# Kernel optimization log

Hardware: AMD Instinct MI355X
Metric: run time of the kernel (lower is better)

Reference implementation:

```python
import jax, jax.numpy as jnp
import numpy as np

L, H, C, V, T_MAX = 12, 12, 768, 50257, 1024
D = C // H
LN_EPS = 1e-5


def layer_norm(x, w, b):
    m = jnp.mean(x, axis=-1, keepdims=True)
    v = jnp.mean(jnp.square(x - m), axis=-1, keepdims=True)
    return (x - m) * jax.lax.rsqrt(v + LN_EPS) * w + b


def setup_inputs() -> dict:
    key = jax.random.key(0)
    ks = jax.random.split(key, 16)
    B, T = 2, 1024
    s = 0.02
    inp = {
        "idx": jax.random.randint(ks[0], (B, T), 0, V),
        "wte": jax.random.normal(ks[1], (V, C), jnp.float32) * s,
        "wpe": jax.random.normal(ks[2], (T_MAX, C), jnp.float32) * s,
        # stacked per-layer params, leading axis = layer
        "ln1_w": jnp.ones((L, C), jnp.float32),
        "ln1_b": jnp.zeros((L, C), jnp.float32),
        "Wq": jax.random.normal(ks[3], (L, C, C), jnp.float32) * s,
        "bq": jnp.zeros((L, C), jnp.float32),
        "Wk": jax.random.normal(ks[4], (L, C, C), jnp.float32) * s,
        "bk": jnp.zeros((L, C), jnp.float32),
        "Wv": jax.random.normal(ks[5], (L, C, C), jnp.float32) * s,
        "bv": jnp.zeros((L, C), jnp.float32),
        "Wo": jax.random.normal(ks[6], (L, C, C), jnp.float32) * (s / np.sqrt(2 * L)),
        "bo": jnp.zeros((L, C), jnp.float32),
        "ln2_w": jnp.ones((L, C), jnp.float32),
        "ln2_b": jnp.zeros((L, C), jnp.float32),
        "Wfc": jax.random.normal(ks[7], (L, C, 4 * C), jnp.float32) * s,
        "bfc": jnp.zeros((L, 4 * C), jnp.float32),
        "Wpr": jax.random.normal(ks[8], (L, 4 * C, C), jnp.float32) * (s / np.sqrt(2 * L)),
        "bpr": jnp.zeros((L, C), jnp.float32),
        "ln_f_w": jnp.ones((C,), jnp.float32),
        "ln_f_b": jnp.zeros((C,), jnp.float32),
        "Wlm": jax.random.normal(ks[9], (C, V), jnp.float32) * s,
    }
    return inp


def _forward(idx, wte, wpe, ln1_w, ln1_b, Wq, bq, Wk, bk, Wv, bv, Wo, bo,
             ln2_w, ln2_b, Wfc, bfc, Wpr, bpr, ln_f_w, ln_f_b, Wlm):
    B, T = idx.shape
    x = wte[idx] + wpe[jnp.arange(T)][None, :, :]  # (B,T,C)
    causal = jnp.tril(jnp.ones((T, T), bool))  # (T,T) causal mask
    scale = 1.0 / np.sqrt(D)
    neg_inf = jnp.finfo(x.dtype).min

    def block(x, p):
        (l1w, l1b, wq, bq_, wk, bk_, wv, bv_, wo, bo_,
         l2w, l2b, wfc, bfc_, wpr, bpr_) = p
        h = layer_norm(x, l1w, l1b)
        q = (h @ wq + bq_).reshape(B, T, H, D)
        k = (h @ wk + bk_).reshape(B, T, H, D)
        v = (h @ wv + bv_).reshape(B, T, H, D)
        scores = jnp.einsum("bqhd,bkhd->bhqk", q, k) * scale
        scores = jnp.where(causal[None, None], scores, neg_inf)
        attn = jax.nn.softmax(scores, axis=-1)
        y = jnp.einsum("bhqk,bkhd->bqhd", attn, v).reshape(B, T, C)
        x = x + y @ wo + bo_
        h2 = layer_norm(x, l2w, l2b)
        x = x + jax.nn.gelu(h2 @ wfc + bfc_, approximate=False) @ wpr + bpr_
        return x, None

    params = (ln1_w, ln1_b, Wq, bq, Wk, bk, Wv, bv, Wo, bo,
              ln2_w, ln2_b, Wfc, bfc, Wpr, bpr)
    x, _ = jax.lax.scan(block, x, params)
    x = layer_norm(x, ln_f_w, ln_f_b)
    logits = x @ Wlm  # (B,T,V)
    return logits


def reference(idx, wte, wpe, ln1_w, ln1_b, Wq, bq, Wk, bk, Wv, bv, Wo, bo,
              ln2_w, ln2_b, Wfc, bfc, Wpr, bpr, ln_f_w, ln_f_b, Wlm):
    return _forward(idx, wte, wpe, ln1_w, ln1_b, Wq, bq, Wk, bk, Wv, bv, Wo, bo,
                    ln2_w, ln2_b, Wfc, bfc, Wpr, bpr, ln_f_w, ln_f_b, Wlm)
```

## Files before the change

### kernel.cpp

```cpp
#include <hip/hip_runtime.h>
#include <math.h>
#include <cstddef>


#define Cdim 768
#define Hn   12
#define Ln   12
#define Tn   1024
#define Bn   2
#define Mrows (Bn * Tn)

typedef unsigned short ushort_t;
typedef __bf16 bf16x8 __attribute__((ext_vector_type(8)));
typedef float  f32x4  __attribute__((ext_vector_type(4)));

__device__ __forceinline__ ushort_t f2bf(float v) {
    union { float f; unsigned int u; } x; x.f = v;
    unsigned int r = x.u + 0x7fffu + ((x.u >> 16) & 1u);
    return (ushort_t)(r >> 16);
}
__device__ __forceinline__ float gelu_f(float v) {
    return 0.5f * v * (1.0f + erff(v * 0.70710678118654752f));
}
__device__ __forceinline__ void gload16(const void* g, void* l) {
    __builtin_amdgcn_global_load_lds(
        (const __attribute__((address_space(1))) unsigned int*)g,
        (__attribute__((address_space(3))) unsigned int*)l, 16, 0, 0);
}

__global__ void embed_k(const int* __restrict__ idx, const float* __restrict__ wte,
                        const float* __restrict__ wpe, float* __restrict__ x) {
    int i = blockIdx.x * 256 + threadIdx.x;
    int c  = i % Cdim;
    int bt = i / Cdim;
    int t  = bt % Tn;
    int tok = idx[bt];
    x[i] = wte[(size_t)tok * Cdim + c] + wpe[(size_t)t * Cdim + c];
}

__global__ __launch_bounds__(256) void ln_k(const float* __restrict__ x,
                                            const float* __restrict__ w,
                                            const float* __restrict__ b,
                                            ushort_t* __restrict__ out) {
    int row = blockIdx.x;
    const float* xr = x + (size_t)row * Cdim;
    int t = threadIdx.x;
    float v0 = xr[t], v1 = xr[t + 256], v2 = xr[t + 512];
    float s = v0 + v1 + v2;
    #pragma unroll
    for (int o = 32; o > 0; o >>= 1) s += __shfl_xor(s, o);
    __shared__ float red[8];
    int wid = t >> 6;
    if ((t & 63) == 0) red[wid] = s;
    __syncthreads();
    float mean = (red[0] + red[1] + red[2] + red[3]) * (1.0f / 768.0f);
    float d0 = v0 - mean, d1 = v1 - mean, d2 = v2 - mean;
    float sq = d0 * d0 + d1 * d1 + d2 * d2;
    #pragma unroll
    for (int o = 32; o > 0; o >>= 1) sq += __shfl_xor(sq, o);
    if ((t & 63) == 0) red[4 + wid] = sq;
    __syncthreads();
    float var = (red[4] + red[5] + red[6] + red[7]) * (1.0f / 768.0f);
    float rstd = rsqrtf(var + 1e-5f);
    ushort_t* orow = out + (size_t)row * Cdim;
    orow[t]       = f2bf(d0 * rstd * w[t]       + b[t]);
    orow[t + 256] = f2bf(d1 * rstd * w[t + 256] + b[t + 256]);
    orow[t + 512] = f2bf(d2 * rstd * w[t + 512] + b[t + 512]);
}

__device__ __forceinline__ void tconv_tile(const float* __restrict__ W,
                                           ushort_t* __restrict__ WT,
                                           int K, int N, int n0, int k0, bool guard) {
    __shared__ float t[32][33];
    int x = threadIdx.x & 31, y = threadIdx.x >> 5;
    #pragma unroll
    for (int j = 0; j < 4; ++j) {
        int kk = k0 + y + j * 8, nn = n0 + x;
        t[y + j * 8][x] = (!guard || nn < N) ? W[(size_t)kk * N + nn] : 0.0f;
    }
    __syncthreads();
    #pragma unroll
    for (int j = 0; j < 4; ++j) {
        int nn = n0 + y + j * 8, kk = k0 + x;
        WT[(size_t)nn * K + kk] = f2bf(t[x][y + j * 8]);
    }
}

__global__ __launch_bounds__(256) void wconv_k(const float* __restrict__ W,
                                               ushort_t* __restrict__ WT,
                                               int K, int N) {
    tconv_tile(W, WT, K, N, blockIdx.x * 32, blockIdx.y * 32, true);
}

__global__ __launch_bounds__(256) void conv_layer_k(
    const float* __restrict__ Wq, const float* __restrict__ Wk,
    const float* __restrict__ Wv, const float* __restrict__ Wo,
    const float* __restrict__ Wfc, const float* __restrict__ Wpr,
    const float* __restrict__ bq, const float* __restrict__ bk,
    const float* __restrict__ bv,
    ushort_t* __restrict__ wqkvt, ushort_t* __restrict__ wot,
    ushort_t* __restrict__ wfct,  ushort_t* __restrict__ wprt,
    float* __restrict__ bqkv) {
    int bid = blockIdx.x;
    if (bid < 2304) {
        int z = bid / 576, t = bid % 576;
        const float* W = (z == 0) ? Wq : (z == 1) ? Wk : (z == 2) ? Wv : Wo;
        ushort_t* dst = (z < 3) ? (wqkvt + (size_t)z * 768 * 768) : wot;
        tconv_tile(W, dst, 768, 768, (t % 24) * 32, (t / 24) * 32, false);
    } else if (bid < 4608) {
        int t = bid - 2304;
        tconv_tile(Wfc, wfct, 768, 3072, (t % 96) * 32, (t / 96) * 32, false);
    } else if (bid < 6912) {
        int t = bid - 4608;
        tconv_tile(Wpr, wprt, 3072, 768, (t % 24) * 32, (t / 24) * 32, false);
    } else {
        int i = (bid - 6912) * 256 + threadIdx.x;
        bqkv[i] = (i < 768) ? bq[i] : (i < 1536 ? bk[i - 768] : bv[i - 1536]);
    }
}

template <bool BIAS, bool GELU_, bool RES, bool OUTBF16>
__global__ __launch_bounds__(256) void gemm_bf16_k(
    const ushort_t* __restrict__ A, const ushort_t* __restrict__ Bt,
    const float* __restrict__ bias, const float* __restrict__ res,
    void* __restrict__ Cout, int M, int N, int K) {
    __shared__ ushort_t Alds[2][128 * 32];
    __shared__ ushort_t Blds[2][128 * 32];
    const int tid = threadIdx.x;
    const int lane = tid & 63;
    const int w = tid >> 6;
    const int wr = w >> 1, wc = w & 1;
    const int m0 = blockIdx.y * 128;
    const int n0 = blockIdx.x * 128;

    f32x4 acc[4][4] = {};
    const int srow = w * 32 + (lane >> 2);
    const int skoff = (lane & 3) * 8;
    const ushort_t* Ab = A  + (size_t)(m0 + srow) * K + skoff;
    const ushort_t* Bb = Bt + (size_t)(n0 + srow) * K + skoff;
    char* Al0 = (char*)&Alds[0][0] + (w * 2048 + lane * 16);
    char* Al1 = (char*)&Alds[1][0] + (w * 2048 + lane * 16);
    char* Bl0 = (char*)&Blds[0][0] + (w * 2048 + lane * 16);
    char* Bl1 = (char*)&Blds[1][0] + (w * 2048 + lane * 16);

    const int nk = K >> 6;
    for (int kb = 0; kb < nk; ++kb) {
        const int k0 = kb << 6;
        __syncthreads();
        gload16(Ab + k0,                       Al0);
        gload16(Ab + k0 + (size_t)16 * K,      Al0 + 1024);
        gload16(Ab + k0 + 32,                  Al1);
        gload16(Ab + k0 + 32 + (size_t)16 * K, Al1 + 1024);
        gload16(Bb + k0,                       Bl0);
        gload16(Bb + k0 + (size_t)16 * K,      Bl0 + 1024);
        gload16(Bb + k0 + 32,                  Bl1);
        gload16(Bb + k0 + 32 + (size_t)16 * K, Bl1 + 1024);
        __syncthreads();
        #pragma unroll
        for (int h = 0; h < 2; ++h) {
            bf16x8 af[4], bfr[4];
            #pragma unroll
            for (int i = 0; i < 4; ++i) {
                af[i]  = *(const bf16x8*)((const char*)&Alds[h][0] +
                           ((wr * 64 + i * 16 + (lane & 15)) * 64 + (lane >> 4) * 16));
                bfr[i] = *(const bf16x8*)((const char*)&Blds[h][0] +
                           ((wc * 64 + i * 16 + (lane & 15)) * 64 + (lane >> 4) * 16));
            }
            #pragma unroll
            for (int mi = 0; mi < 4; ++mi)
                #pragma unroll
                for (int ni = 0; ni < 4; ++ni)
                    acc[mi][ni] = __builtin_amdgcn_mfma_f32_16x16x32_bf16(
                        af[mi], bfr[ni], acc[mi][ni], 0, 0, 0);
        }
    }
    const int r0 = (lane >> 4) * 4;
    const int c0 = lane & 15;
    #pragma unroll
    for (int mi = 0; mi < 4; ++mi) {
        #pragma unroll
        for (int ni = 0; ni < 4; ++ni) {
            int col = n0 + wc * 64 + ni * 16 + c0;
            if (col < N) {
                #pragma unroll
                for (int q = 0; q < 4; ++q) {
                    int row = m0 + wr * 64 + mi * 16 + r0 + q;
                    float v = acc[mi][ni][q];
                    if (BIAS) v += bias[col];
                    if (GELU_) v = gelu_f(v);
                    if (RES) v += res[(size_t)row * N + col];
                    if (OUTBF16) ((ushort_t*)Cout)[(size_t)row * N + col] = f2bf(v);
                    else         ((float*)Cout)[(size_t)row * N + col] = v;
                }
            }
        }
    }
}

__global__ __launch_bounds__(512, 2) void gemm_lm_k(
    const ushort_t* __restrict__ A,
    const ushort_t* __restrict__ Bt,
    float* __restrict__ Cout,
    int M, int N, int K, int cpx) {
    __shared__ ushort_t Asl[2][256 * 64];
    __shared__ ushort_t Bsl[2][256 * 64];
    const int tid = threadIdx.x;
    const int lane = tid & 63;
    const int w = tid >> 6;
    const int wr = w >> 2, wc = w & 3;
    const int lid = ((int)blockIdx.x & 7) * cpx + ((int)blockIdx.x >> 3);
    const int m0 = (lid & 7) * 256;
    const int n0 = (lid >> 3) * 256;

    f32x4 acc[8][4] = {};

    const int srow = tid >> 3;
    const int scol = ((tid & 7) * 8) ^ (((tid >> 5) & 1) << 4);
    const ushort_t* Asrc = A  + (size_t)(m0 + srow) * K + scol;
    const ushort_t* Bsrc = Bt + (size_t)(n0 + srow) * K + scol;
    const int ldsoff = tid * 16;

    const int nt = K >> 6;
    #pragma unroll
    for (int j = 0; j < 4; ++j) {
        gload16(Asrc + (size_t)(j * 64) * K, (char*)&Asl[0][0] + ldsoff + j * 8192);
        gload16(Bsrc + (size_t)(j * 64) * K, (char*)&Bsl[0][0] + ldsoff + j * 8192);
    }
    for (int t = 0; t < nt; ++t) {
        const int buf = t & 1;
        if (t + 1 < nt) {
            const int k0 = (t + 1) << 6;
            #pragma unroll
            for (int j = 0; j < 4; ++j) {
                gload16(Asrc + k0 + (size_t)(j * 64) * K,
                        (char*)&Asl[buf ^ 1][0] + ldsoff + j * 8192);
                gload16(Bsrc + k0 + (size_t)(j * 64) * K,
                        (char*)&Bsl[buf ^ 1][0] + ldsoff + j * 8192);
            }
            asm volatile("s_waitcnt vmcnt(8)" ::: "memory");
        } else {
            asm volatile("s_waitcnt vmcnt(0)" ::: "memory");
        }
        __builtin_amdgcn_sched_barrier(0);
        __builtin_amdgcn_s_barrier();
        asm volatile("" ::: "memory");

        const char* Ab = (const char*)&Asl[buf][0];
        const char* Bb = (const char*)&Bsl[buf][0];
        bf16x8 bfr[4][2];
        #pragma unroll
        for (int n = 0; n < 4; ++n)
            #pragma unroll
            for (int ks = 0; ks < 2; ++ks) {
                int row = wc * 64 + n * 16 + (lane & 15);
                int o = row * 128 + ks * 64 + ((lane >> 4) * 16);
                o ^= ((row >> 2) & 1) << 5;
                bfr[n][ks] = *(const bf16x8*)(Bb + o);
            }
        __builtin_amdgcn_s_setprio(1);
        #pragma unroll
        for (int m = 0; m < 8; ++m) {
            bf16x8 af[2];
            #pragma unroll
            for (int ks = 0; ks < 2; ++ks) {
                int row = wr * 128 + m * 16 + (lane & 15);
                int o = row * 128 + ks * 64 + ((lane >> 4) * 16);
                o ^= ((row >> 2) & 1) << 5;
                af[ks] = *(const bf16x8*)(Ab + o);
            }
            #pragma unroll
            for (int n = 0; n < 4; ++n)
                #pragma unroll
                for (int ks = 0; ks < 2; ++ks)
                    acc[m][n] = __builtin_amdgcn_mfma_f32_16x16x32_bf16(
                        af[ks], bfr[n][ks], acc[m][n], 0, 0, 0);
        }
        __builtin_amdgcn_s_setprio(0);
        asm volatile("" ::: "memory");
        __builtin_amdgcn_sched_barrier(0);
        __builtin_amdgcn_s_barrier();
    }

    const int r0 = (lane >> 4) * 4, c0 = lane & 15;
    #pragma unroll
    for (int m = 0; m < 8; ++m)
        #pragma unroll
        for (int n = 0; n < 4; ++n) {
            int col = n0 + wc * 64 + n * 16 + c0;
            if (col < N) {
                #pragma unroll
                for (int q = 0; q < 4; ++q) {
                    int row = m0 + wr * 128 + m * 16 + r0 + q;
                    Cout[(size_t)row * N + col] = acc[m][n][q];
                }
            }
        }
}

template <bool BIAS, bool RES>
__global__ __launch_bounds__(256) void gemm64_k(
    const ushort_t* __restrict__ A, const ushort_t* __restrict__ Bt,
    const float* __restrict__ bias, const float* __restrict__ res,
    float* __restrict__ Cout, int M, int N, int K) {
    __shared__ ushort_t Alds[4][64 * 32];
    __shared__ ushort_t Blds[4][64 * 32];
    const int tid = threadIdx.x;
    const int lane = tid & 63;
    const int w = tid >> 6;
    const int wr = w >> 1, wc = w & 1;
    const int m0 = blockIdx.y * 64;
    const int n0 = blockIdx.x * 64;

    f32x4 acc[2][2] = {};
    const int srow = w * 16 + (lane >> 2);
    const int skoff = (lane & 3) * 8;
    const ushort_t* Ab = A  + (size_t)(m0 + srow) * K + skoff;
    const ushort_t* Bb = Bt + (size_t)(n0 + srow) * K + skoff;

    const int nk = K >> 7;
    for (int kb = 0; kb < nk; ++kb) {
        const int k0 = kb << 7;
        __syncthreads();
        #pragma unroll
        for (int s = 0; s < 4; ++s) {
            gload16(Ab + k0 + s * 32, (char*)&Alds[s][0] + (w * 1024 + lane * 16));
            gload16(Bb + k0 + s * 32, (char*)&Blds[s][0] + (w * 1024 + lane * 16));
        }
        __syncthreads();
        #pragma unroll
        for (int s = 0; s < 4; ++s) {
            bf16x8 af[2], bfr[2];
            #pragma unroll
            for (int i = 0; i < 2; ++i) {
                af[i]  = *(const bf16x8*)((const char*)&Alds[s][0] +
                           ((wr * 32 + i * 16 + (lane & 15)) * 64 + (lane >> 4) * 16));
                bfr[i] = *(const bf16x8*)((const char*)&Blds[s][0] +
                           ((wc * 32 + i * 16 + (lane & 15)) * 64 + (lane >> 4) * 16));
            }
            #pragma unroll
            for (int mi = 0; mi < 2; ++mi)
                #pragma unroll
                for (int ni = 0; ni < 2; ++ni)
                    acc[mi][ni] = __builtin_amdgcn_mfma_f32_16x16x32_bf16(
                        af[mi], bfr[ni], acc[mi][ni], 0, 0, 0);
        }
    }
    const int r0 = (lane >> 4) * 4;
    const int c0 = lane & 15;
    #pragma unroll
    for (int mi = 0; mi < 2; ++mi)
        #pragma unroll
        for (int ni = 0; ni < 2; ++ni) {
            int col = n0 + wc * 32 + ni * 16 + c0;
            #pragma unroll
            for (int q = 0; q < 4; ++q) {
                int row = m0 + wr * 32 + mi * 16 + r0 + q;
                float v = acc[mi][ni][q];
                if (BIAS) v += bias[col];
                if (RES) v += res[(size_t)row * N + col];
                Cout[(size_t)row * N + col] = v;
            }
        }
}

__global__ __launch_bounds__(256) void kvprep_k(const ushort_t* __restrict__ qkvb,
                                                ushort_t* __restrict__ kpb,
                                                ushort_t* __restrict__ vtb) {
    __shared__ ushort_t Ls[256][72];
    const int tc = blockIdx.x, h = blockIdx.y, b = blockIdx.z;
    const int tid = threadIdx.x;
    const int tok = tc * 256 + tid;
    const ushort_t* base = qkvb + (size_t)(b * Tn + tok) * 2304 + h * 64;
    ushort_t* kdst = kpb + ((size_t)(b * Hn + h) * Tn + tok) * 64;
    #pragma unroll
    for (int i = 0; i < 8; ++i)
        *(uint4*)&kdst[i * 8] = *(const uint4*)(base + 768 + i * 8);
    #pragma unroll
    for (int i = 0; i < 8; ++i)
        *(uint4*)&Ls[tid][i * 8] = *(const uint4*)(base + 1536 + i * 8);
    __syncthreads();
    const int d = tid & 63, tg = tid >> 6;
    ushort_t tmp[64];
    #pragma unroll
    for (int i = 0; i < 64; ++i) tmp[i] = Ls[tg * 64 + i][d];
    ushort_t* dst = vtb + ((size_t)(b * Hn + h) * 64 + d) * Tn + tc * 256 + tg * 64;
    #pragma unroll
    for (int i = 0; i < 8; ++i)
        *(uint4*)&dst[i * 8] = *(const uint4*)&tmp[i * 8];
}

__global__ __launch_bounds__(256) void attn_mfma_k(
    const ushort_t* __restrict__ qkvb,
    const ushort_t* __restrict__ kpb,
    const ushort_t* __restrict__ vtb,
    ushort_t* __restrict__ yb) {
    __shared__ ushort_t Ks[64][72];
    __shared__ ushort_t Vt[64][72];
    __shared__ ushort_t Pl[4][16][72];
    const int chunk = (Tn / 64 - 1) - blockIdx.x;
    const int h = blockIdx.y, b = blockIdx.z;
    const int tid = threadIdx.x, lane = tid & 63, w = tid >> 6;
    const int c = lane & 15, g = lane >> 4;
    const int qrow0 = chunk * 64 + w * 16;

    const ushort_t* qp = qkvb + (size_t)(b * Tn + qrow0 + c) * 2304 + h * 64 + g * 8;
    bf16x8 qa0 = *(const bf16x8*)qp;
    bf16x8 qa1 = *(const bf16x8*)(qp + 32);

    f32x4 accO[4] = {};
    float mrun[4], lrun[4];
    #pragma unroll
    for (int q = 0; q < 4; ++q) { mrun[q] = -1e30f; lrun[q] = 0.0f; }

    const int skey = tid >> 2, sd0 = (tid & 3) * 16;
    const ushort_t* ksrc = kpb + ((size_t)(b * Hn + h) * Tn + skey) * 64 + sd0;
    const int vd = tid >> 2, vseg = tid & 3;
    const ushort_t* vsrc = vtb + ((size_t)(b * Hn + h) * 64 + vd) * Tn + vseg * 16;
    ushort_t* KsW = &Ks[skey][sd0];
    ushort_t* VtW = &Vt[vd][vseg * 16];

    const int ntiles = chunk + 1;
    for (int kt = 0; kt < ntiles; ++kt) {
        __syncthreads();
        {
            const ushort_t* kp = ksrc + (size_t)kt * 64 * 64;
            *(uint4*)KsW       = *(const uint4*)kp;
            *(uint4*)(KsW + 8) = *(const uint4*)(kp + 8);
            const ushort_t* vp = vsrc + kt * 64;
            *(uint4*)VtW       = *(const uint4*)vp;
            *(uint4*)(VtW + 8) = *(const uint4*)(vp + 8);
        }
        __syncthreads();

        f32x4 sf[4];
        #pragma unroll
        for (int nk = 0; nk < 4; ++nk) {
            bf16x8 kf0 = *(const bf16x8*)&Ks[nk * 16 + c][g * 8];
            bf16x8 kf1 = *(const bf16x8*)&Ks[nk * 16 + c][g * 8 + 32];
            f32x4 z = {};
            z = __builtin_amdgcn_mfma_f32_16x16x32_bf16(qa0, kf0, z, 0, 0, 0);
            z = __builtin_amdgcn_mfma_f32_16x16x32_bf16(qa1, kf1, z, 0, 0, 0);
            sf[nk] = z;
        }
        float pmax[4] = {-1e30f, -1e30f, -1e30f, -1e30f};
        #pragma unroll
        for (int nk = 0; nk < 4; ++nk) {
            int key = kt * 64 + nk * 16 + c;
            #pragma unroll
            for (int q = 0; q < 4; ++q) {
                float sv = sf[nk][q];
                int row = qrow0 + g * 4 + q;
                sv = (key > row) ? -1e30f : sv;
                sf[nk][q] = sv;
                pmax[q] = fmaxf(pmax[q], sv);
            }
        }
        #pragma unroll
        for (int q = 0; q < 4; ++q)
            #pragma unroll
            for (int off = 1; off < 16; off <<= 1)
                pmax[q] = fmaxf(pmax[q], __shfl_xor(pmax[q], off));
        float corr[4], psum[4];
        #pragma unroll
        for (int q = 0; q < 4; ++q) {
            float mn = fmaxf(mrun[q], pmax[q]);
            corr[q] = __expf((mrun[q] - mn) * 0.125f);
            mrun[q] = mn;
            psum[q] = 0.0f;
        }
        #pragma unroll
        for (int nk = 0; nk < 4; ++nk)
            #pragma unroll
            for (int q = 0; q < 4; ++q) {
                float p = __expf((sf[nk][q] - mrun[q]) * 0.125f);
                psum[q] += p;
                Pl[w][g * 4 + q][nk * 16 + c] = f2bf(p);
            }
        #pragma unroll
        for (int q = 0; q < 4; ++q) {
            #pragma unroll
            for (int off = 1; off < 16; off <<= 1)
                psum[q] += __shfl_xor(psum[q], off);
            lrun[q] = lrun[q] * corr[q] + psum[q];
        }
        #pragma unroll
        for (int ni = 0; ni < 4; ++ni)
            #pragma unroll
            for (int q = 0; q < 4; ++q)
                accO[ni][q] *= corr[q];

        asm volatile("" ::: "memory");
        bf16x8 pa0 = *(const bf16x8*)&Pl[w][c][g * 8];
        bf16x8 pa1 = *(const bf16x8*)&Pl[w][c][g * 8 + 32];
        #pragma unroll
        for (int ni = 0; ni < 4; ++ni) {
            bf16x8 bv0 = *(const bf16x8*)&Vt[ni * 16 + c][g * 8];
            bf16x8 bv1 = *(const bf16x8*)&Vt[ni * 16 + c][g * 8 + 32];
            accO[ni] = __builtin_amdgcn_mfma_f32_16x16x32_bf16(pa0, bv0, accO[ni], 0, 0, 0);
            accO[ni] = __builtin_amdgcn_mfma_f32_16x16x32_bf16(pa1, bv1, accO[ni], 0, 0, 0);
        }
    }

    #pragma unroll
    for (int q = 0; q < 4; ++q) {
        float inv = 1.0f / lrun[q];
        ushort_t* yr = yb + (size_t)(b * Tn + qrow0 + g * 4 + q) * Cdim + h * 64;
        #pragma unroll
        for (int ni = 0; ni < 4; ++ni)
            yr[ni * 16 + c] = f2bf(accO[ni][q] * inv);
    }
}

extern "C" void kernel_launch(void* const* d_in, const int* in_sizes, int n_in,
                              void* d_out, int out_size, void* d_ws, size_t ws_size,
                              hipStream_t stream) {
    const int*   idx  = (const int*)d_in[0];
    const float* wte  = (const float*)d_in[1];
    const float* wpe  = (const float*)d_in[2];
    const float* ln1w = (const float*)d_in[3];
    const float* ln1b = (const float*)d_in[4];
    const float* Wq   = (const float*)d_in[5];
    const float* bq   = (const float*)d_in[6];
    const float* Wk   = (const float*)d_in[7];
    const float* bk   = (const float*)d_in[8];
    const float* Wv   = (const float*)d_in[9];
    const float* bv   = (const float*)d_in[10];
    const float* Wo   = (const float*)d_in[11];
    const float* bo   = (const float*)d_in[12];
    const float* ln2w = (const float*)d_in[13];
    const float* ln2b = (const float*)d_in[14];
    const float* Wfc  = (const float*)d_in[15];
    const float* bfc  = (const float*)d_in[16];
    const float* Wpr  = (const float*)d_in[17];
    const float* bpr  = (const float*)d_in[18];
    const float* lnfw = (const float*)d_in[19];
    const float* lnfb = (const float*)d_in[20];
    const float* Wlm  = (const float*)d_in[21];
    float* out = (float*)d_out;

    const int M = Mrows;
    const int V = out_size / M;
    const int Vpad = ((V + 255) / 256) * 256;

    float*    x     = (float*)d_ws;
    float*    bqkv  = x + (size_t)M * Cdim;
    ushort_t* qkvb  = (ushort_t*)(bqkv + 2304);
    ushort_t* kpb   = qkvb + (size_t)M * 2304;
    ushort_t* vtb   = kpb + (size_t)Bn * Hn * Tn * 64;
    ushort_t* hb    = vtb + (size_t)Bn * Hn * 64 * Tn;
    ushort_t* yb    = hb + (size_t)M * Cdim;
    ushort_t* mid   = yb + (size_t)M * Cdim;
    ushort_t* wqkvt = mid + (size_t)M * 3072;
    ushort_t* wot   = wqkvt + (size_t)2304 * Cdim;
    ushort_t* wfct  = wot + (size_t)Cdim * Cdim;
    ushort_t* wprt  = wfct + (size_t)3072 * Cdim;
    ushort_t* wlmt  = wprt + (size_t)Cdim * 3072;

    embed_k<<<(M * Cdim) / 256, 256, 0, stream>>>(idx, wte, wpe, x);

    for (int l = 0; l < Ln; ++l) {
        const size_t wo2 = (size_t)l * Cdim * Cdim;
        const size_t wo4 = (size_t)l * Cdim * 4 * Cdim;
        conv_layer_k<<<6921, 256, 0, stream>>>(
            Wq + wo2, Wk + wo2, Wv + wo2, Wo + wo2, Wfc + wo4, Wpr + wo4,
            bq + l * Cdim, bk + l * Cdim, bv + l * Cdim,
            wqkvt, wot, wfct, wprt, bqkv);

        ln_k<<<M, 256, 0, stream>>>(x, ln1w + l * Cdim, ln1b + l * Cdim, hb);
        gemm_bf16_k<true, false, false, true><<<dim3(18, 16), 256, 0, stream>>>(
            hb, wqkvt, bqkv, nullptr, qkvb, M, 2304, Cdim);
        kvprep_k<<<dim3(4, Hn, Bn), 256, 0, stream>>>(qkvb, kpb, vtb);
        attn_mfma_k<<<dim3(16, Hn, Bn), 256, 0, stream>>>(qkvb, kpb, vtb, yb);
        gemm64_k<true, true><<<dim3(12, 32), 256, 0, stream>>>(
            yb, wot, bo + l * Cdim, x, x, M, Cdim, Cdim);
        ln_k<<<M, 256, 0, stream>>>(x, ln2w + l * Cdim, ln2b + l * Cdim, hb);
        gemm_bf16_k<true, true, false, true><<<dim3(24, 16), 256, 0, stream>>>(
            hb, wfct, bfc + (size_t)l * 4 * Cdim, nullptr, mid, M, 3072, Cdim);
        gemm64_k<true, true><<<dim3(12, 32), 256, 0, stream>>>(
            mid, wprt, bpr + l * Cdim, x, x, M, Cdim, 3072);
    }

    ln_k<<<M, 256, 0, stream>>>(x, lnfw, lnfb, hb);
    wconv_k<<<dim3(Vpad / 32, 24), 256, 0, stream>>>(Wlm, wlmt, Cdim, V);
    const int nblk = (Vpad / 256) * 8;
    gemm_lm_k<<<nblk, 512, 0, stream>>>(hb, wlmt, out, M, V, Cdim, nblk / 8);
}
```

Before: 2.195 ms.

## Interleave LM-head GEMM global prefetch with MFMA phases using XOR-swizzled LDS

```diff
diff --git a/kernel.cpp b/kernel.cpp
--- a/kernel.cpp
+++ b/kernel.cpp
@@ -202,8 +202,9 @@
     const ushort_t* __restrict__ Bt,
     float* __restrict__ Cout,
     int M, int N, int K, int cpx) {
-    __shared__ ushort_t Asl[2][256 * 64];
-    __shared__ ushort_t Bsl[2][256 * 64];
+    __shared__ char lds[131072];
+    char* Abase = lds;
+    char* Bbase = lds + 65536;
     const int tid = threadIdx.x;
     const int lane = tid & 63;
     const int w = tid >> 6;
@@ -214,71 +215,82 @@
 
     f32x4 acc[8][4] = {};
 
-    const int srow = tid >> 3;
-    const int scol = ((tid & 7) * 8) ^ (((tid >> 5) & 1) << 4);
-    const ushort_t* Asrc = A  + (size_t)(m0 + srow) * K + scol;
-    const ushort_t* Bsrc = Bt + (size_t)(n0 + srow) * K + scol;
-    const int ldsoff = tid * 16;
+    const int srowl = tid >> 3;
+    const int sslot = (tid & 7) ^ (srowl & 7);
+    const ushort_t* Asrc = A  + (size_t)(m0 + srowl) * K + sslot * 8;
+    const ushort_t* Bsrc = Bt + (size_t)(n0 + srowl) * K + sslot * 8;
+    const int ldst = tid * 16;
+
+    auto stage = [&](int d, int ht, int kt) {
+        int h = ht & 1;
+        if (ht < 2) {
+            gload16(Asrc + (size_t)(h * 128) * K + kt * 64,
+                    Abase + d * 32768 + h * 16384 + ldst);
+            gload16(Asrc + (size_t)(h * 128 + 64) * K + kt * 64,
+                    Abase + d * 32768 + h * 16384 + 8192 + ldst);
+        } else {
+            gload16(Bsrc + (size_t)(h * 128) * K + kt * 64,
+                    Bbase + d * 32768 + h * 16384 + ldst);
+            gload16(Bsrc + (size_t)(h * 128 + 64) * K + kt * 64,
+                    Bbase + d * 32768 + h * 16384 + 8192 + ldst);
+        }
+    };
+    auto readA = [&](int d, int m, int ks) -> bf16x8 {
+        int rl = m * 16 + (lane & 15);
+        int s  = ks * 4 + (lane >> 4);
+        return *(const bf16x8*)(Abase + d * 32768 + wr * 16384 + rl * 128 +
+                                ((s ^ (rl & 7)) << 4));
+    };
+    auto readB = [&](int d, int n, int ks) -> bf16x8 {
+        int rl = (wc & 1) * 64 + n * 16 + (lane & 15);
+        int s  = ks * 4 + (lane >> 4);
+        return *(const bf16x8*)(Bbase + d * 32768 + (wc >> 1) * 16384 + rl * 128 +
+                                ((s ^ (rl & 7)) << 4));
+    };
 
     const int nt = K >> 6;
     #pragma unroll
-    for (int j = 0; j < 4; ++j) {
-        gload16(Asrc + (size_t)(j * 64) * K, (char*)&Asl[0][0] + ldsoff + j * 8192);
-        gload16(Bsrc + (size_t)(j * 64) * K, (char*)&Bsl[0][0] + ldsoff + j * 8192);
-    }
-    for (int t = 0; t < nt; ++t) {
-        const int buf = t & 1;
-        if (t + 1 < nt) {
-            const int k0 = (t + 1) << 6;
-            #pragma unroll
-            for (int j = 0; j < 4; ++j) {
-                gload16(Asrc + k0 + (size_t)(j * 64) * K,
-                        (char*)&Asl[buf ^ 1][0] + ldsoff + j * 8192);
-                gload16(Bsrc + k0 + (size_t)(j * 64) * K,
-                        (char*)&Bsl[buf ^ 1][0] + ldsoff + j * 8192);
-            }
-            asm volatile("s_waitcnt vmcnt(8)" ::: "memory");
-        } else {
-            asm volatile("s_waitcnt vmcnt(0)" ::: "memory");
-        }
-        __builtin_amdgcn_sched_barrier(0);
-        __builtin_amdgcn_s_barrier();
-        asm volatile("" ::: "memory");
-
-        const char* Ab = (const char*)&Asl[buf][0];
-        const char* Bb = (const char*)&Bsl[buf][0];
+    for (int ht = 0; ht < 4; ++ht) stage(0, ht, 0);
+
+    for (int kt = 0; kt < nt; ++kt) {
+        const int d = kt & 1;
         bf16x8 bfr[4][2];
         #pragma unroll
-        for (int n = 0; n < 4; ++n)
-            #pragma unroll
-            for (int ks = 0; ks < 2; ++ks) {
-                int row = wc * 64 + n * 16 + (lane & 15);
-                int o = row * 128 + ks * 64 + ((lane >> 4) * 16);
-                o ^= ((row >> 2) & 1) << 5;
-                bfr[n][ks] = *(const bf16x8*)(Bb + o);
-            }
-        __builtin_amdgcn_s_setprio(1);
-        #pragma unroll
-        for (int m = 0; m < 8; ++m) {
-            bf16x8 af[2];
-            #pragma unroll
-            for (int ks = 0; ks < 2; ++ks) {
-                int row = wr * 128 + m * 16 + (lane & 15);
-                int o = row * 128 + ks * 64 + ((lane >> 4) * 16);
-                o ^= ((row >> 2) & 1) << 5;
-                af[ks] = *(const bf16x8*)(Ab + o);
-            }
-            #pragma unroll
-            for (int n = 0; n < 4; ++n)
-                #pragma unroll
-                for (int ks = 0; ks < 2; ++ks)
-                    acc[m][n] = __builtin_amdgcn_mfma_f32_16x16x32_bf16(
-                        af[ks], bfr[n][ks], acc[m][n], 0, 0, 0);
-        }
-        __builtin_amdgcn_s_setprio(0);
-        asm volatile("" ::: "memory");
-        __builtin_amdgcn_sched_barrier(0);
-        __builtin_amdgcn_s_barrier();
+        for (int p = 0; p < 4; ++p) {
+            if (kt + 1 < nt) stage(d ^ 1, p, kt + 1);
+            if (p == 0) {
+                if (kt + 1 < nt) asm volatile("s_waitcnt vmcnt(2)" ::: "memory");
+                else             asm volatile("s_waitcnt vmcnt(0)" ::: "memory");
+            }
+            __builtin_amdgcn_s_barrier();
+            asm volatile("" ::: "memory");
+            if (p == 0) {
+                #pragma unroll
+                for (int n = 0; n < 4; ++n)
+                    #pragma unroll
+                    for (int ks = 0; ks < 2; ++ks) bfr[n][ks] = readB(d, n, ks);
+            }
+            bf16x8 af[2][2];
+            #pragma unroll
+            for (int mm = 0; mm < 2; ++mm)
+                #pragma unroll
+                for (int ks = 0; ks < 2; ++ks) af[mm][ks] = readA(d, p * 2 + mm, ks);
+            asm volatile("s_waitcnt lgkmcnt(0)" ::: "memory");
+            __builtin_amdgcn_sched_barrier(0);
+            __builtin_amdgcn_s_setprio(1);
+            #pragma unroll
+            for (int mm = 0; mm < 2; ++mm)
+                #pragma unroll
+                for (int n = 0; n < 4; ++n)
+                    #pragma unroll
+                    for (int ks = 0; ks < 2; ++ks)
+                        acc[p * 2 + mm][n] = __builtin_amdgcn_mfma_f32_16x16x32_bf16(
+                            af[mm][ks], bfr[n][ks], acc[p * 2 + mm][n], 0, 0, 0);
+            __builtin_amdgcn_s_setprio(0);
+            __builtin_amdgcn_sched_barrier(0);
+            asm volatile("" ::: "memory");
+            __builtin_amdgcn_s_barrier();
+        }
     }
 
     const int r0 = (lane >> 4) * 4, c0 = lane & 15;
```

Measured after the change: 2.165 ms. Within noise of the previous version (-1.4%).
